# Optimization experiments

Measured on AMD Instinct MI355X. Metric: run time of the kernel, lower is better.

Reference implementation:

```python
import jax, jax.numpy as jnp
import numpy as np

PRE_NMS_TOPK = 6000
POST_NMS_TOPK = 1000
NMS_THRESH = 0.7
MIN_SIZE = 16.0
N = 1_000_000
H, W = 800, 1333


def setup_inputs() -> dict:
    key = jax.random.key(0)
    ki, kx, ky, kw, kh, kd, kl = jax.random.split(key, 7)
    image = jax.random.normal(ki, (1, H, W, 3), jnp.float32)
    # realistic anchors: centers uniform over image, sizes in [8, 228)
    cx = jax.random.uniform(kx, (N,), jnp.float32) * W
    cy = jax.random.uniform(ky, (N,), jnp.float32) * H
    aw = jax.random.uniform(kw, (N,), jnp.float32) * 220.0 + 8.0
    ah = jax.random.uniform(kh, (N,), jnp.float32) * 220.0 + 8.0
    anchors = jnp.stack([cx - 0.5 * aw, cy - 0.5 * ah, cx + 0.5 * aw, cy + 0.5 * ah], axis=1)
    bbox_deltas = jax.random.normal(kd, (N, 4), jnp.float32) * 0.1
    logits = jax.random.normal(kl, (N, 1), jnp.float32)
    return {"image": image, "anchors": anchors, "bbox_deltas": bbox_deltas, "logits": logits}


def _iou_matrix(boxes):
    # boxes: [K,4] as (x1,y1,x2,y2); IoU is symmetric in axis labeling,
    # matching tf.image.non_max_suppression's overlap math.
    x1, y1, x2, y2 = boxes[:, 0], boxes[:, 1], boxes[:, 2], boxes[:, 3]
    area = (x2 - x1) * (y2 - y1)
    ix1 = jnp.maximum(x1[:, None], x1[None, :])
    iy1 = jnp.maximum(y1[:, None], y1[None, :])
    ix2 = jnp.minimum(x2[:, None], x2[None, :])
    iy2 = jnp.minimum(y2[:, None], y2[None, :])
    inter = jnp.maximum(ix2 - ix1, 0.0) * jnp.maximum(iy2 - iy1, 0.0)
    union = area[:, None] + area[None, :] - inter
    return jnp.where(union > 0.0, inter / union, 0.0)


def _sequential_nms(iou, valid, thresh):
    # iou: [K,K]; boxes are already sorted by descending score.
    K = iou.shape[0]
    idx = jnp.arange(K)

    def step(keep, inp):
        i, row = inp
        ki = keep[i]
        suppress = ki & (row > thresh) & (idx > i)
        return keep & ~suppress, ki

    _, kept = jax.lax.scan(step, valid, (idx, iou))
    return kept  # [K] bool, in sorted order


def reference(image, anchors, bbox_deltas, logits):
    height = jnp.float32(image.shape[1])
    width = jnp.float32(image.shape[2])

    # --- box decode ---
    wa = anchors[:, 2] - anchors[:, 0]
    ha = anchors[:, 3] - anchors[:, 1]
    xa = anchors[:, 0] + 0.5 * wa
    ya = anchors[:, 1] + 0.5 * ha
    x = bbox_deltas[:, 0] * wa + xa
    y = bbox_deltas[:, 1] * ha + ya
    w = jnp.exp(bbox_deltas[:, 2]) * wa
    h = jnp.exp(bbox_deltas[:, 3]) * ha
    x1 = jnp.clip(x - 0.5 * w, 0.0, width - 1.0)
    y1 = jnp.clip(y - 0.5 * h, 0.0, height - 1.0)
    x2 = jnp.clip(x + 0.5 * w, 0.0, width - 1.0)
    y2 = jnp.clip(y + 0.5 * h, 0.0, height - 1.0)
    proposals = jnp.stack([x1, y1, x2, y2], axis=1)  # [N,4]

    # --- min-size filter (mask instead of dynamic gather) ---
    valid = ((x2 - x1) >= MIN_SIZE) & ((y2 - y1) >= MIN_SIZE)
    scores = jnp.where(valid, jax.nn.sigmoid(logits[:, 0]), -jnp.inf)

    # --- pre-NMS top-k ---
    top_scores, top_idx = jax.lax.top_k(scores, PRE_NMS_TOPK)
    top_boxes = proposals[top_idx]              # [K,4]
    top_valid = top_scores > -jnp.inf

    # --- NMS ---
    iou = _iou_matrix(top_boxes)
    kept = _sequential_nms(iou, top_valid, NMS_THRESH)

    # --- pack kept boxes (in score order) into fixed [POST,4], zero-padded ---
    rank = jnp.cumsum(kept.astype(jnp.int32)) - 1
    slot = jnp.where(kept, rank, POST_NMS_TOPK)  # invalid -> dropped
    out = jnp.zeros((POST_NMS_TOPK, 4), top_boxes.dtype)
    out = out.at[slot].set(top_boxes, mode="drop")
    return out
```

## Files before the change

### kernel.cpp

```cpp
#include <hip/hip_runtime.h>
#include <stdint.h>
#include <math.h>

#define N_ANCH   1000000
#define N4       (N_ANCH / 4)
#define NBLK4    ((N4 + 1023) / 1024)
#define PRE_K    6000
#define POST_K   1000
#define WORDS    94
#define ROWS     6016
#define W_IMG    1333.0f
#define H_IMG    800.0f

#define NS       7168
#define RBLK     112

#define OFF_KEYS   0x000000u
#define OFF_HIST1  0x400000u
#define OFF_HIST2  0x404000u
#define OFF_CTRL   0x410000u
#define OFF_CAND   0x410100u
#define OFF_BOXES  0x41F000u
#define OFF_VALID  0x437000u
#define OFF_MASK   0x440000u

__device__ __forceinline__ float ref_exp(float v) {
  return (float)exp((double)v);
}

__device__ __forceinline__ void decode_box(float ax, float ay, float az, float aw,
                                           float dx, float dy, float dz, float dw,
                                           float& x1, float& y1, float& x2, float& y2,
                                           bool& valid) {
  float wa = __fsub_rn(az, ax);
  float ha = __fsub_rn(aw, ay);
  float xa = __fadd_rn(ax, __fmul_rn(0.5f, wa));
  float ya = __fadd_rn(ay, __fmul_rn(0.5f, ha));
  float x  = __fadd_rn(__fmul_rn(dx, wa), xa);
  float y  = __fadd_rn(__fmul_rn(dy, ha), ya);
  float w  = __fmul_rn(ref_exp(dz), wa);
  float h  = __fmul_rn(ref_exp(dw), ha);
  float hw = __fmul_rn(0.5f, w);
  float hh = __fmul_rn(0.5f, h);
  x1 = fminf(fmaxf(__fsub_rn(x, hw), 0.0f), W_IMG - 1.0f);
  y1 = fminf(fmaxf(__fsub_rn(y, hh), 0.0f), H_IMG - 1.0f);
  x2 = fminf(fmaxf(__fadd_rn(x, hw), 0.0f), W_IMG - 1.0f);
  y2 = fminf(fmaxf(__fadd_rn(y, hh), 0.0f), H_IMG - 1.0f);
  valid = (__fsub_rn(x2, x1) >= 16.0f) && (__fsub_rn(y2, y1) >= 16.0f);
}

__device__ __forceinline__ uint32_t wave_iscan(uint32_t x, int lane) {
  #pragma unroll
  for (int off = 1; off < 64; off <<= 1) {
    uint32_t u = __shfl_up(x, off, 64);
    if (lane >= off) x += u;
  }
  return x;
}

__device__ __forceinline__ uint64_t bcast64(uint64_t v, int lane) {
  uint32_t lo = (uint32_t)__builtin_amdgcn_readlane((int)(uint32_t)v, lane);
  uint32_t hi = (uint32_t)__builtin_amdgcn_readlane((int)(uint32_t)(v >> 32), lane);
  return ((uint64_t)hi << 32) | lo;
}

__device__ __forceinline__ void findcut1_dev(const uint32_t* __restrict__ hist1,
                                             uint32_t& c_out, uint32_t& base_out) {
  __shared__ uint32_t part[1024];
  __shared__ uint32_t s_c, s_base;
  int t = threadIdx.x;
  if (t == 0) { s_c = 4095u; s_base = 0u; }
  uint4 s4 = ((const uint4*)hist1)[t];
  uint32_t tot = s4.x + s4.y + s4.z + s4.w;
  part[t] = tot;
  __syncthreads();
  uint32_t inc = tot;
  for (int off = 1; off < 1024; off <<= 1) {
    uint32_t u = (t >= off) ? part[t - off] : 0u;
    __syncthreads();
    inc += u;
    part[t] = inc;
    __syncthreads();
  }
  uint32_t ex = inc - tot;
  if (ex < PRE_K && inc >= PRE_K) {
    uint32_t run = ex;
    uint32_t binv[4] = { s4.x, s4.y, s4.z, s4.w };
    for (int b = 0; b < 4; b++) {
      if (run + binv[b] >= PRE_K) { s_c = 4 * t + b; s_base = run; break; }
      run += binv[b];
    }
  }
  if (t == 1023 && inc < PRE_K) { s_c = 4095u; s_base = inc; }
  __syncthreads();
  c_out = s_c; base_out = s_base;
}

__device__ __forceinline__ uint32_t findcut2_dev(const uint32_t* __restrict__ hist2,
                                                 uint32_t c, uint32_t base) {
  __shared__ uint32_t s_T;
  int t = threadIdx.x;
  if (t == 0) s_T = 0xFFFFFu;
  __syncthreads();
  if (t < 64) {
    int lane = t;
    const uint32_t* p = hist2 + 4 * lane;
    uint32_t b0 = p[0], b1 = p[1], b2 = p[2], b3 = p[3];
    uint32_t tot = b0 + b1 + b2 + b3;
    uint32_t inc = wave_iscan(tot, lane);
    uint32_t ex = inc - tot;
    if (base + ex < PRE_K && base + inc >= PRE_K) {
      uint32_t run = base + ex;
      uint32_t binv[4] = { b0, b1, b2, b3 };
      for (int b = 0; b < 4; b++) {
        if (run + binv[b] >= PRE_K) { s_T = (c << 8) | (uint32_t)(4 * lane + b); break; }
        run += binv[b];
      }
    }
  }
  __syncthreads();
  return s_T;
}

__global__ void __launch_bounds__(256) k_decode(const float4* __restrict__ anchors,
                                                const float4* __restrict__ deltas,
                                                const float*  __restrict__ logits,
                                                uint32_t* __restrict__ keys) {
  int i = blockIdx.x * 256 + threadIdx.x;
  if (i >= N_ANCH) return;
  float4 a = anchors[i];
  float4 d = deltas[i];
  float wa = a.z - a.x, ha = a.w - a.y;
  float xa = a.x + 0.5f * wa, ya = a.y + 0.5f * ha;
  float x = d.x * wa + xa, y = d.y * ha + ya;
  float w = __expf(d.z) * wa, h = __expf(d.w) * ha;
  float fx1 = fminf(fmaxf(x - 0.5f * w, 0.0f), W_IMG - 1.0f);
  float fx2 = fminf(fmaxf(x + 0.5f * w, 0.0f), W_IMG - 1.0f);
  float fy1 = fminf(fmaxf(y - 0.5f * h, 0.0f), H_IMG - 1.0f);
  float fy2 = fminf(fmaxf(y + 0.5f * h, 0.0f), H_IMG - 1.0f);
  float X = fx2 - fx1, Y = fy2 - fy1;
  bool valid = (X >= 16.0f) && (Y >= 16.0f);
  if (fabsf(X - 16.0f) < 0.02f || fabsf(Y - 16.0f) < 0.02f) {
    float ex1, ey1, ex2, ey2; bool vv;
    decode_box(a.x, a.y, a.z, a.w, d.x, d.y, d.z, d.w, ex1, ey1, ex2, ey2, vv);
    valid = vv;
  }
  uint32_t u = __float_as_uint(logits[i]);
  uint32_t o = (u & 0x80000000u) ? ~u : (u | 0x80000000u);
  keys[i] = valid ? ~o : 0xFFFFFFFFu;
}

__global__ void __launch_bounds__(1024) k_histA(const uint4* __restrict__ keys4,
                                                uint32_t* __restrict__ hist1) {
  __shared__ uint32_t lh[4096];
  int tid = threadIdx.x, lane = tid & 63;
  for (int b = tid; b < 4096; b += 1024) lh[b] = 0u;
  __syncthreads();
  int i4 = blockIdx.x * 1024 + tid;
  uint32_t invc = 0;
  if (i4 < N4) {
    uint4 kk = keys4[i4];
    uint32_t ks[4] = { kk.x, kk.y, kk.z, kk.w };
    #pragma unroll
    for (int e = 0; e < 4; e++) {
      if (ks[e] != 0xFFFFFFFFu) atomicAdd(&lh[ks[e] >> 20], 1u);
      else invc++;
    }
  }
  #pragma unroll
  for (int off = 32; off > 0; off >>= 1) invc += __shfl_down(invc, off, 64);
  if (lane == 0 && invc) atomicAdd(&lh[4095], invc);
  __syncthreads();
  for (int b = tid; b < 4096; b += 1024) {
    uint32_t cv = lh[b];
    if (cv) atomicAdd(&hist1[b], cv);
  }
}

__global__ void __launch_bounds__(1024) k_hist2(const uint4* __restrict__ keys4,
                                                const uint32_t* __restrict__ hist1,
                                                uint32_t* __restrict__ hist2) {
  uint32_t c, base;
  findcut1_dev(hist1, c, base);
  __shared__ uint32_t lh[256];
  int tid = threadIdx.x;
  if (tid < 256) lh[tid] = 0u;
  __syncthreads();
  int i4 = blockIdx.x * 1024 + tid;
  if (i4 < N4) {
    uint4 kk = keys4[i4];
    uint32_t ks[4] = { kk.x, kk.y, kk.z, kk.w };
    #pragma unroll
    for (int e = 0; e < 4; e++)
      if ((ks[e] >> 20) == c) atomicAdd(&lh[(ks[e] >> 12) & 0xFFu], 1u);
  }
  __syncthreads();
  if (tid < 256) {
    uint32_t v = lh[tid];
    if (v) atomicAdd(&hist2[tid], v);
  }
}

__global__ void __launch_bounds__(1024) k_compact(const uint4* __restrict__ keys4,
                                                  const float* __restrict__ logits,
                                                  const uint32_t* __restrict__ hist1,
                                                  const uint32_t* __restrict__ hist2,
                                                  uint32_t* __restrict__ cnt,
                                                  uint64_t* __restrict__ cand) {
  uint32_t c, base;
  findcut1_dev(hist1, c, base);
  uint32_t T = findcut2_dev(hist2, c, base);
  int tid = threadIdx.x, lane = tid & 63;
  int i4 = blockIdx.x * 1024 + tid;
  uint4 kk = make_uint4(~0u, ~0u, ~0u, ~0u);
  if (i4 < N4) kk = keys4[i4];
  uint32_t ks[4] = { kk.x, kk.y, kk.z, kk.w };
  #pragma unroll
  for (int e = 0; e < 4; e++) {
    bool pass = (i4 < N4) && ((ks[e] >> 12) <= T);
    uint64_t m = __ballot(pass);
    if (pass) {
      int i = 4 * i4 + e;
      uint32_t skey;
      if (ks[e] == 0xFFFFFFFFu) {
        skey = 0xFF800000u;
      } else {
        double xd = (double)logits[i];
        float s = (float)(1.0 / (1.0 + exp(-xd)));
        skey = 0x7FFFFFFFu & ~__float_as_uint(s);
      }
      int leader = __ffsll((unsigned long long)m) - 1;
      uint32_t bpos = 0;
      if (lane == leader) bpos = atomicAdd(cnt, (uint32_t)__popcll((unsigned long long)m));
      bpos = (uint32_t)__shfl((int)bpos, leader);
      uint32_t pos = (uint32_t)__popcll((unsigned long long)(m & ((1ull << lane) - 1ull)));
      uint32_t p = bpos + pos;
      if (p < NS) cand[p] = ((uint64_t)skey << 20) | (uint32_t)i;
    }
  }
}

__global__ void __launch_bounds__(256) k_rank(
    const uint32_t* __restrict__ ctrl,
    const uint64_t* __restrict__ cand,
    const float4* __restrict__ anchors,
    const float4* __restrict__ deltas,
    float4* __restrict__ boxes,
    uint32_t* __restrict__ valid) {
  __shared__ uint32_t part[4][64];
  int tid = threadIdx.x;
  int wv = tid >> 6, lane = tid & 63;
  int i = blockIdx.x * 64 + lane;
  uint32_t M = ctrl[0]; if (M > NS) M = NS;
  uint64_t myk = (i < (int)M) ? cand[i] : ~0ull;
  uint32_t cnt = 0;
  const int QUART = NS / 4;
  int jbase = wv * QUART;
  for (int s = 0; s < QUART / 64; s++) {
    int j = jbase + s * 64 + lane;
    uint64_t c = (j < (int)M) ? cand[j] : ~0ull;
    #pragma unroll
    for (int s2 = 0; s2 < 64; s2++) {
      uint64_t kb = bcast64(c, s2);
      cnt += (kb < myk) ? 1u : 0u;
    }
  }
  part[wv][lane] = cnt;
  __syncthreads();
  if (wv != 0) return;
  uint32_t rank = part[0][lane] + part[1][lane] + part[2][lane] + part[3][lane];
  if (i < (int)M && rank < PRE_K) {
    uint32_t skey = (uint32_t)(myk >> 20);
    uint32_t idx  = (uint32_t)(myk & 0xFFFFFu);
    if (skey >= 0xFF800000u) {
      boxes[rank] = make_float4(0.f, 0.f, 0.f, 0.f);
      valid[rank] = 0u;
    } else {
      float4 a = anchors[idx];
      float4 d = deltas[idx];
      float x1, y1, x2, y2; bool vv;
      decode_box(a.x, a.y, a.z, a.w, d.x, d.y, d.z, d.w, x1, y1, x2, y2, vv);
      boxes[rank] = make_float4(x1, y1, x2, y2);
      valid[rank] = 1u;
    }
  }
  if ((i >= (int)M || i >= PRE_K) && i < ROWS) {
    boxes[i] = make_float4(0.f, 0.f, 0.f, 0.f);
    valid[i] = 0u;
  }
}

__global__ void __launch_bounds__(64) k_iou(const float4* __restrict__ boxes,
                                            uint64_t* __restrict__ mask) {
  int by = blockIdx.y, bx = blockIdx.x;
  if (bx < by) return;
  __shared__ float4 cb[64];
  int t = threadIdx.x;
  cb[t] = boxes[bx * 64 + t];
  __syncthreads();
  int i = by * 64 + t;
  float4 b = boxes[i];
  float ax1 = b.x, ay1 = b.y, ax2 = b.z, ay2 = b.w;
  float areaA = __fmul_rn(__fsub_rn(ax2, ax1), __fsub_rn(ay2, ay1));
  uint64_t bits = 0;
  for (int c = 0; c < 64; c++) {
    float4 o = cb[c];
    float areaB = __fmul_rn(__fsub_rn(o.z, o.x), __fsub_rn(o.w, o.y));
    float ix1 = fmaxf(ax1, o.x), iy1 = fmaxf(ay1, o.y);
    float ix2 = fminf(ax2, o.z), iy2 = fminf(ay2, o.w);
    float iw = fmaxf(__fsub_rn(ix2, ix1), 0.0f);
    float ih = fmaxf(__fsub_rn(iy2, iy1), 0.0f);
    float inter = __fmul_rn(iw, ih);
    float uni = __fsub_rn(__fadd_rn(areaA, areaB), inter);
    bool sup = (uni > 0.0f) && (__fdiv_rn(inter, uni) > 0.7f);
    bits |= ((uint64_t)sup) << c;
  }
  mask[(size_t)i * WORDS + bx] = bits;
}

__global__ void __launch_bounds__(64, 1) k_nms(const uint64_t* __restrict__ mask,
                                               const float4* __restrict__ boxes,
                                               const uint32_t* __restrict__ valid,
                                               float* __restrict__ out) {
  __shared__ uint32_t list[1088];
  int lane = threadIdx.x;
  int wp = (2 * lane < WORDS) ? 2 * lane : 0;
  uint64_t rA = 0, rB = 0;
  int cnt = 0;
  uint64_t colv = mask[(size_t)lane * WORDS + 0];
  uint32_t vf = valid[lane];
  for (int g = 0; g < WORDS; g++) {
    int base = g * 64;
    uint64_t vA[64], vB[64];
    #pragma unroll
    for (int r = 0; r < 64; r++) {
      ulonglong2 t2 = *(const ulonglong2*)(mask + (size_t)(base + r) * WORDS + wp);
      vA[r] = t2.x; vB[r] = t2.y;
    }
    uint64_t colv_c = colv;
    uint32_t vf_c = vf;
    if (g + 1 < WORDS) {
      colv = mask[(size_t)(base + 64 + lane) * WORDS + (g + 1)];
      vf = valid[base + 64 + lane];
    }
    uint64_t cur = (g & 1) ? bcast64(rB, g >> 1) : bcast64(rA, g >> 1);
    uint64_t vmask = __ballot(vf_c != 0u);
    uint64_t alive = vmask & ~cur;
    uint64_t kept = 0;
    #pragma unroll
    for (int r = 0; r < 64; r++) {
      uint64_t mr = bcast64(colv_c, r);
      uint64_t take = (alive >> r) & 1ull;
      kept |= take << r;
      alive &= ~(take ? mr : 0ull);
    }
    uint32_t below = (uint32_t)__popcll((unsigned long long)(kept & ((1ull << lane) - 1ull)));
    if ((kept >> lane) & 1ull) {
      uint32_t pos = (uint32_t)cnt + below;
      if (pos < 1088u) list[pos] = (uint32_t)(base + lane);
    }
    cnt += (int)__popcll((unsigned long long)kept);
    if (cnt >= POST_K) break;
    if (g + 1 >= WORDS) break;
    uint64_t accA = 0, accB = 0;
    #pragma unroll
    for (int r = 0; r < 64; r++) {
      uint64_t s = 0ull - ((kept >> r) & 1ull);
      accA |= vA[r] & s;
      accB |= vB[r] & s;
    }
    rA |= accA;
    rB |= accB;
  }
  __syncthreads();
  float4* outv = (float4*)out;
  for (int k = lane; k < POST_K; k += 64)
    outv[k] = (k < cnt) ? boxes[list[k]] : make_float4(0.f, 0.f, 0.f, 0.f);
}

extern "C" void kernel_launch(void* const* d_in, const int* in_sizes, int n_in,
                              void* d_out, int out_size, void* d_ws, size_t ws_size,
                              hipStream_t stream) {
  const float4* anchors = (const float4*)d_in[1];
  const float4* deltas  = (const float4*)d_in[2];
  const float*  logits  = (const float*)d_in[3];
  char* w = (char*)d_ws;
  uint32_t* keys  = (uint32_t*)(w + OFF_KEYS);
  uint32_t* hist1 = (uint32_t*)(w + OFF_HIST1);
  uint32_t* hist2 = (uint32_t*)(w + OFF_HIST2);
  uint32_t* ctrl  = (uint32_t*)(w + OFF_CTRL);
  uint64_t* cand  = (uint64_t*)(w + OFF_CAND);
  float4*   boxes = (float4*)(w + OFF_BOXES);
  uint32_t* valid = (uint32_t*)(w + OFF_VALID);
  uint64_t* mask  = (uint64_t*)(w + OFF_MASK);
  float*    out   = (float*)d_out;

  hipMemsetAsync(w + OFF_HIST1, 0, 0x4400, stream);
  hipMemsetAsync(w + OFF_CTRL, 0, 256, stream);

  k_decode<<<(N_ANCH + 255) / 256, 256, 0, stream>>>(anchors, deltas, logits, keys);
  k_histA<<<NBLK4, 1024, 0, stream>>>((const uint4*)keys, hist1);
  k_hist2<<<NBLK4, 1024, 0, stream>>>((const uint4*)keys, hist1, hist2);
  k_compact<<<NBLK4, 1024, 0, stream>>>((const uint4*)keys, logits, hist1, hist2, &ctrl[0], cand);
  k_rank<<<RBLK, 256, 0, stream>>>(ctrl, cand, anchors, deltas, boxes, valid);
  k_iou<<<dim3(WORDS, WORDS), 64, 0, stream>>>(boxes, mask);
  k_nms<<<1, 64, 0, stream>>>(mask, boxes, valid, out);
}
```

Measured before the change: 279.8 us.

## Hoist radix cut search into single-block kernels and shrink compaction blocks

The prefix-scan cut search over the histograms, previously repeated redundantly in every block of k_hist2 and k_compact, moves into two tiny single-block kernels (k_cut1, k_cut2) that write their results to a control buffer. The hist2 and compact passes then read those thresholds and run with 256-thread blocks instead of 1024. Compaction now reserves output slots with one atomic per block instead of one per wave per element. This trades two extra kernel launches for removing about 250 redundant 1024-wide block scans with many __syncthreads, and cuts contention on the global counter.

```diff
diff --git a/kernel.cpp b/kernel.cpp
--- a/kernel.cpp
+++ b/kernel.cpp
@@ -5,6 +5,7 @@
 #define N_ANCH   1000000
 #define N4       (N_ANCH / 4)
 #define NBLK4    ((N4 + 1023) / 1024)
+#define NBLK256  ((N4 + 255) / 256)
 #define PRE_K    6000
 #define POST_K   1000
 #define WORDS    94
@@ -62,64 +63,6 @@
   uint32_t lo = (uint32_t)__builtin_amdgcn_readlane((int)(uint32_t)v, lane);
   uint32_t hi = (uint32_t)__builtin_amdgcn_readlane((int)(uint32_t)(v >> 32), lane);
   return ((uint64_t)hi << 32) | lo;
-}
-
-__device__ __forceinline__ void findcut1_dev(const uint32_t* __restrict__ hist1,
-                                             uint32_t& c_out, uint32_t& base_out) {
-  __shared__ uint32_t part[1024];
-  __shared__ uint32_t s_c, s_base;
-  int t = threadIdx.x;
-  if (t == 0) { s_c = 4095u; s_base = 0u; }
-  uint4 s4 = ((const uint4*)hist1)[t];
-  uint32_t tot = s4.x + s4.y + s4.z + s4.w;
-  part[t] = tot;
-  __syncthreads();
-  uint32_t inc = tot;
-  for (int off = 1; off < 1024; off <<= 1) {
-    uint32_t u = (t >= off) ? part[t - off] : 0u;
-    __syncthreads();
-    inc += u;
-    part[t] = inc;
-    __syncthreads();
-  }
-  uint32_t ex = inc - tot;
-  if (ex < PRE_K && inc >= PRE_K) {
-    uint32_t run = ex;
-    uint32_t binv[4] = { s4.x, s4.y, s4.z, s4.w };
-    for (int b = 0; b < 4; b++) {
-      if (run + binv[b] >= PRE_K) { s_c = 4 * t + b; s_base = run; break; }
-      run += binv[b];
-    }
-  }
-  if (t == 1023 && inc < PRE_K) { s_c = 4095u; s_base = inc; }
-  __syncthreads();
-  c_out = s_c; base_out = s_base;
-}
-
-__device__ __forceinline__ uint32_t findcut2_dev(const uint32_t* __restrict__ hist2,
-                                                 uint32_t c, uint32_t base) {
-  __shared__ uint32_t s_T;
-  int t = threadIdx.x;
-  if (t == 0) s_T = 0xFFFFFu;
-  __syncthreads();
-  if (t < 64) {
-    int lane = t;
-    const uint32_t* p = hist2 + 4 * lane;
-    uint32_t b0 = p[0], b1 = p[1], b2 = p[2], b3 = p[3];
-    uint32_t tot = b0 + b1 + b2 + b3;
-    uint32_t inc = wave_iscan(tot, lane);
-    uint32_t ex = inc - tot;
-    if (base + ex < PRE_K && base + inc >= PRE_K) {
-      uint32_t run = base + ex;
-      uint32_t binv[4] = { b0, b1, b2, b3 };
-      for (int b = 0; b < 4; b++) {
-        if (run + binv[b] >= PRE_K) { s_T = (c << 8) | (uint32_t)(4 * lane + b); break; }
-        run += binv[b];
-      }
-    }
-  }
-  __syncthreads();
-  return s_T;
 }
 
 __global__ void __launch_bounds__(256) k_decode(const float4* __restrict__ anchors,
@@ -177,16 +120,43 @@
   }
 }
 
-__global__ void __launch_bounds__(1024) k_hist2(const uint4* __restrict__ keys4,
-                                                const uint32_t* __restrict__ hist1,
-                                                uint32_t* __restrict__ hist2) {
-  uint32_t c, base;
-  findcut1_dev(hist1, c, base);
+__global__ void __launch_bounds__(1024) k_cut1(const uint32_t* __restrict__ hist1,
+                                               uint32_t* __restrict__ ctrl) {
+  __shared__ uint32_t part[1024];
+  int t = threadIdx.x;
+  uint4 s4 = ((const uint4*)hist1)[t];
+  uint32_t tot = s4.x + s4.y + s4.z + s4.w;
+  part[t] = tot;
+  __syncthreads();
+  uint32_t inc = tot;
+  for (int off = 1; off < 1024; off <<= 1) {
+    uint32_t u = (t >= off) ? part[t - off] : 0u;
+    __syncthreads();
+    inc += u;
+    part[t] = inc;
+    __syncthreads();
+  }
+  uint32_t ex = inc - tot;
+  if (ex < PRE_K && inc >= PRE_K) {
+    uint32_t run = ex;
+    uint32_t binv[4] = { s4.x, s4.y, s4.z, s4.w };
+    for (int b = 0; b < 4; b++) {
+      if (run + binv[b] >= PRE_K) { ctrl[2] = 4 * t + b; ctrl[3] = run; break; }
+      run += binv[b];
+    }
+  }
+  if (t == 1023 && inc < PRE_K) { ctrl[2] = 4095u; ctrl[3] = inc; }
+}
+
+__global__ void __launch_bounds__(256) k_hist2(const uint4* __restrict__ keys4,
+                                               const uint32_t* __restrict__ ctrl,
+                                               uint32_t* __restrict__ hist2) {
   __shared__ uint32_t lh[256];
   int tid = threadIdx.x;
-  if (tid < 256) lh[tid] = 0u;
-  __syncthreads();
-  int i4 = blockIdx.x * 1024 + tid;
+  lh[tid] = 0u;
+  __syncthreads();
+  uint32_t c = ctrl[2];
+  int i4 = blockIdx.x * 256 + tid;
   if (i4 < N4) {
     uint4 kk = keys4[i4];
     uint32_t ks[4] = { kk.x, kk.y, kk.z, kk.w };
@@ -195,31 +165,65 @@
       if ((ks[e] >> 20) == c) atomicAdd(&lh[(ks[e] >> 12) & 0xFFu], 1u);
   }
   __syncthreads();
-  if (tid < 256) {
-    uint32_t v = lh[tid];
-    if (v) atomicAdd(&hist2[tid], v);
-  }
-}
-
-__global__ void __launch_bounds__(1024) k_compact(const uint4* __restrict__ keys4,
-                                                  const float* __restrict__ logits,
-                                                  const uint32_t* __restrict__ hist1,
-                                                  const uint32_t* __restrict__ hist2,
-                                                  uint32_t* __restrict__ cnt,
-                                                  uint64_t* __restrict__ cand) {
-  uint32_t c, base;
-  findcut1_dev(hist1, c, base);
-  uint32_t T = findcut2_dev(hist2, c, base);
-  int tid = threadIdx.x, lane = tid & 63;
-  int i4 = blockIdx.x * 1024 + tid;
+  uint32_t v = lh[tid];
+  if (v) atomicAdd(&hist2[tid], v);
+}
+
+__global__ void __launch_bounds__(64) k_cut2(const uint32_t* __restrict__ hist2,
+                                             uint32_t* __restrict__ ctrl) {
+  int lane = threadIdx.x;
+  uint32_t c = ctrl[2], base = ctrl[3];
+  const uint32_t* p = hist2 + 4 * lane;
+  uint32_t b0 = p[0], b1 = p[1], b2 = p[2], b3 = p[3];
+  uint32_t tot = b0 + b1 + b2 + b3;
+  uint32_t inc = wave_iscan(tot, lane);
+  uint32_t ex = inc - tot;
+  bool found = false;
+  if (base + ex < PRE_K && base + inc >= PRE_K) {
+    uint32_t run = base + ex;
+    uint32_t binv[4] = { b0, b1, b2, b3 };
+    for (int b = 0; b < 4; b++) {
+      if (run + binv[b] >= PRE_K) { ctrl[1] = (c << 8) | (uint32_t)(4 * lane + b); found = true; break; }
+      run += binv[b];
+    }
+  }
+  uint64_t fb = __ballot(found);
+  if (lane == 0 && fb == 0ull) ctrl[1] = 0xFFFFFu;
+}
+
+__global__ void __launch_bounds__(256) k_compact(const uint4* __restrict__ keys4,
+                                                 const float* __restrict__ logits,
+                                                 uint32_t* ctrl,
+                                                 uint64_t* __restrict__ cand) {
+  __shared__ uint32_t wcnt[4];
+  __shared__ uint32_t bbase_s;
+  int tid = threadIdx.x, lane = tid & 63, wv = tid >> 6;
+  uint32_t T = ctrl[1];
+  int i4 = blockIdx.x * 256 + tid;
   uint4 kk = make_uint4(~0u, ~0u, ~0u, ~0u);
   if (i4 < N4) kk = keys4[i4];
   uint32_t ks[4] = { kk.x, kk.y, kk.z, kk.w };
+  bool pass[4]; uint64_t m[4];
+  uint32_t tot = 0;
   #pragma unroll
   for (int e = 0; e < 4; e++) {
-    bool pass = (i4 < N4) && ((ks[e] >> 12) <= T);
-    uint64_t m = __ballot(pass);
-    if (pass) {
+    pass[e] = (i4 < N4) && ((ks[e] >> 12) <= T);
+    m[e] = __ballot(pass[e]);
+    tot += (uint32_t)__popcll((unsigned long long)m[e]);
+  }
+  if (lane == 0) wcnt[wv] = tot;
+  __syncthreads();
+  if (tid == 0) {
+    uint32_t bt = wcnt[0] + wcnt[1] + wcnt[2] + wcnt[3];
+    bbase_s = bt ? atomicAdd(&ctrl[0], bt) : 0u;
+  }
+  __syncthreads();
+  uint32_t wb = bbase_s;
+  for (int w2 = 0; w2 < wv; w2++) wb += wcnt[w2];
+  uint64_t lmask = (1ull << lane) - 1ull;
+  #pragma unroll
+  for (int e = 0; e < 4; e++) {
+    if (pass[e]) {
       int i = 4 * i4 + e;
       uint32_t skey;
       if (ks[e] == 0xFFFFFFFFu) {
@@ -229,14 +233,10 @@
         float s = (float)(1.0 / (1.0 + exp(-xd)));
         skey = 0x7FFFFFFFu & ~__float_as_uint(s);
       }
-      int leader = __ffsll((unsigned long long)m) - 1;
-      uint32_t bpos = 0;
-      if (lane == leader) bpos = atomicAdd(cnt, (uint32_t)__popcll((unsigned long long)m));
-      bpos = (uint32_t)__shfl((int)bpos, leader);
-      uint32_t pos = (uint32_t)__popcll((unsigned long long)(m & ((1ull << lane) - 1ull)));
-      uint32_t p = bpos + pos;
+      uint32_t p = wb + (uint32_t)__popcll((unsigned long long)(m[e] & lmask));
       if (p < NS) cand[p] = ((uint64_t)skey << 20) | (uint32_t)i;
     }
+    wb += (uint32_t)__popcll((unsigned long long)m[e]);
   }
 }
 
@@ -400,8 +400,10 @@
 
   k_decode<<<(N_ANCH + 255) / 256, 256, 0, stream>>>(anchors, deltas, logits, keys);
   k_histA<<<NBLK4, 1024, 0, stream>>>((const uint4*)keys, hist1);
-  k_hist2<<<NBLK4, 1024, 0, stream>>>((const uint4*)keys, hist1, hist2);
-  k_compact<<<NBLK4, 1024, 0, stream>>>((const uint4*)keys, logits, hist1, hist2, &ctrl[0], cand);
+  k_cut1<<<1, 1024, 0, stream>>>(hist1, ctrl);
+  k_hist2<<<NBLK256, 256, 0, stream>>>((const uint4*)keys, ctrl, hist2);
+  k_cut2<<<1, 64, 0, stream>>>(hist2, ctrl);
+  k_compact<<<NBLK256, 256, 0, stream>>>((const uint4*)keys, logits, ctrl, cand);
   k_rank<<<RBLK, 256, 0, stream>>>(ctrl, cand, anchors, deltas, boxes, valid);
   k_iou<<<dim3(WORDS, WORDS), 64, 0, stream>>>(boxes, mask);
   k_nms<<<1, 64, 0, stream>>>(mask, boxes, valid, out);
```

Result: faster. 239.5 us (-14.4%).
